# Kernel optimization log

Hardware: AMD Instinct MI355X
Metric: run time of the kernel (lower is better)

## Reference

```python
import jax, jax.numpy as jnp
import numpy as np

RADIUS = 4  # matches init radius


def _bilinear_sample(v, grid):
    """Faithful F.grid_sample(v, grid, mode='bilinear', align_corners=True, padding_mode='zeros').
    v: (B,C,H,W); grid: (B,Hg,Wg,2) in [-1,1]; grid[...,0]->width(x), grid[...,1]->height(y)."""
    B, C, H, W = v.shape
    Hg, Wg = grid.shape[1], grid.shape[2]
    ix = (grid[..., 0] + 1.0) * 0.5 * (W - 1)
    iy = (grid[..., 1] + 1.0) * 0.5 * (H - 1)
    x0 = jnp.floor(ix); y0 = jnp.floor(iy)
    x1 = x0 + 1.0;      y1 = y0 + 1.0
    wx1 = ix - x0; wx0 = 1.0 - wx1
    wy1 = iy - y0; wy0 = 1.0 - wy1
    v_flat = v.reshape(B, C, H * W)
    out = jnp.zeros((B, C, Hg, Wg), v.dtype)
    for xf, yf, w in ((x0, y0, wx0 * wy0), (x1, y0, wx1 * wy0),
                      (x0, y1, wx0 * wy1), (x1, y1, wx1 * wy1)):
        valid = (xf >= 0) & (xf <= W - 1) & (yf >= 0) & (yf <= H - 1)
        xi = jnp.clip(xf, 0, W - 1).astype(jnp.int32)
        yi = jnp.clip(yf, 0, H - 1).astype(jnp.int32)
        idx = (yi * W + xi).reshape(B, 1, Hg * Wg)
        g = jnp.take_along_axis(v_flat, idx, axis=2).reshape(B, C, Hg, Wg)
        out = out + g * (w * valid)[:, None, :, :]
    return out


def setup_inputs() -> dict:
    key = jax.random.key(0)
    ks = jax.random.split(key, 5)
    B, C, H, W, K = 4, 128, 128, 128, 8
    x = jax.random.normal(ks[0], (B, C, H, W), jnp.float32)
    psf_tbl = jax.random.randint(ks[1], (B, H, W, K, 2), 0, 128)  # absolute pixel anchors
    delta = jax.random.normal(ks[2], (1, 1, 1, K, 2), jnp.float32) * 0.1
    w_qkv = jax.random.normal(ks[3], (3 * C, C), jnp.float32) * (C ** -0.5)  # 1x1 conv, no bias
    w_proj = jax.random.normal(ks[4], (C, C), jnp.float32) * (C ** -0.5)
    return {"x": x, "psf_tbl": psf_tbl, "delta": delta, "w_qkv": w_qkv, "w_proj": w_proj}


def reference(x, psf_tbl, delta, w_qkv, w_proj):
    B, C, H, W = x.shape
    K = psf_tbl.shape[3]
    qkv = jnp.einsum('oc,bchw->bohw', w_qkv, x)  # 1x1 conv to_qkv
    q, k, v = jnp.split(qkv, 3, axis=1)
    offsets = psf_tbl.astype(x.dtype) + jnp.tanh(delta) * RADIUS  # (B,H,W,K,2)
    norm = jnp.array([H - 1, W - 1], x.dtype)
    grid = (offsets / norm * 2.0 - 1.0).reshape(B, H, W * K, 2)
    k_s = _bilinear_sample(k, grid).reshape(B, C, H, W, K)
    v_s = _bilinear_sample(v, grid).reshape(B, C, H, W, K)
    attn = jnp.einsum('bchw,bchwk->bhwk', q, k_s) * (C ** -0.5)
    attn = jax.nn.softmax(attn, axis=-1)  # softmax over K sampled points
    out = jnp.einsum('bhwk,bchwk->bchw', attn, v_s)
    return x + jnp.einsum('oc,bchw->bohw', w_proj, out)
```

## Files before the change

kernel.cpp:

```cpp
#include <hip/hip_runtime.h>

#define HW 16384
#define C 128

typedef __attribute__((ext_vector_type(8))) short short8;
typedef __attribute__((ext_vector_type(4))) float f32x4;
typedef __attribute__((ext_vector_type(2))) float f32x2;

__device__ __forceinline__ unsigned short f2bf(float f) {
  union { float f; unsigned u; } v; v.f = f;
  return (unsigned short)((v.u + 0x7fffu + ((v.u >> 16) & 1u)) >> 16);
}
#if __has_builtin(__builtin_amdgcn_cvt_pk_bf16_f32)
typedef __attribute__((ext_vector_type(2))) __bf16 bf16x2;
__device__ __forceinline__ unsigned pk2(float a, float b) {
  union { bf16x2 v; unsigned u; } cv;
  cv.v = __builtin_amdgcn_cvt_pk_bf16_f32(a, b);
  return cv.u;
}
#else
__device__ __forceinline__ unsigned pk2(float a, float b) {
  return (unsigned)f2bf(a) | ((unsigned)f2bf(b) << 16);
}
#endif
__device__ __forceinline__ unsigned short f2bf1(float a) {
  return (unsigned short)(pk2(a, a) & 0xffffu);
}
__device__ __forceinline__ float bflo(unsigned w) {
  union { unsigned u; float f; } v; v.u = w << 16; return v.f;
}
__device__ __forceinline__ float bfhi(unsigned w) {
  union { unsigned u; float f; } v; v.u = w & 0xffff0000u; return v.f;
}

__global__ void k_prep(const float* __restrict__ delta, float* __restrict__ pw,
                       int* __restrict__ pi) {
  int k = threadIdx.x;
  if (k < 8) {
    float s0 = tanhf(delta[k * 2 + 0]) * 4.0f;
    float s1 = tanhf(delta[k * 2 + 1]) * 4.0f;
    float f0 = floorf(s0), f1 = floorf(s1);
    pi[2 * k + 0] = (int)f0;
    pi[2 * k + 1] = (int)f1;
    float fx = s0 - f0, fy = s1 - f1;
    pw[4 * k + 0] = (1.0f - fx) * (1.0f - fy);
    pw[4 * k + 1] = fx * (1.0f - fy);
    pw[4 * k + 2] = (1.0f - fx) * fy;
    pw[4 * k + 3] = fx * fy;
  }
}

__global__ __launch_bounds__(256) void k_qkv(const float* __restrict__ x,
                                             const float* __restrict__ w_qkv,
                                             unsigned short* __restrict__ qb,
                                             unsigned* __restrict__ kvb) {
  __shared__ __align__(16) unsigned char smem[66560];
  unsigned short* Xs = (unsigned short*)smem;
  unsigned short* Ws = (unsigned short*)(smem + 32768);
  const int t = threadIdx.x;
  const int gpix0 = blockIdx.x * 128;
  const int b = gpix0 >> 14;
  const int hw0 = gpix0 & (HW - 1);

  const float* xb = x + (size_t)b * C * HW + hw0;
  #pragma unroll
  for (int i = 0; i < 16; ++i) {
    int linear = i * 256 + t;
    int p = linear & 127;
    int c4 = (linear >> 7) * 4;
    float a0 = xb[(size_t)(c4 + 0) * HW + p];
    float a1 = xb[(size_t)(c4 + 1) * HW + p];
    float a2 = xb[(size_t)(c4 + 2) * HW + p];
    float a3 = xb[(size_t)(c4 + 3) * HW + p];
    int cc = c4 ^ ((p & 7) << 3);
    *(uint2*)&Xs[p * 128 + cc] = make_uint2(pk2(a0, a1), pk2(a2, a3));
  }

  const int wave = t >> 6, lane = t & 63;
  const int wr = wave >> 1, wc = wave & 1;
  const int rsel = lane & 15, quad = lane >> 4;

  #pragma unroll
  for (int i = 0; i < 16; ++i) {
    int linear = i * 256 + t;
    int c4 = (linear & 31) * 4;
    int o = linear >> 5;
    float4 w4 = *(const float4*)(w_qkv + (size_t)o * C + c4);
    *(uint2*)&Ws[o * 128 + (c4 ^ ((o & 7) << 3))] = make_uint2(pk2(w4.x, w4.y), pk2(w4.z, w4.w));
  }
  __syncthreads();
  {
    f32x4 acc[4][4];
    #pragma unroll
    for (int mi = 0; mi < 4; ++mi)
      #pragma unroll
      for (int ni = 0; ni < 4; ++ni) acc[mi][ni] = (f32x4){0.f, 0.f, 0.f, 0.f};
    #pragma unroll
    for (int ks = 0; ks < 4; ++ks) {
      const int koff = ks * 32 + quad * 8;
      short8 afr[4], bfr[4];
      #pragma unroll
      for (int mi = 0; mi < 4; ++mi) {
        int r = wr * 64 + mi * 16 + rsel;
        afr[mi] = *(const short8*)&Xs[r * 128 + (koff ^ ((r & 7) << 3))];
      }
      #pragma unroll
      for (int ni = 0; ni < 4; ++ni) {
        int r = wc * 64 + ni * 16 + rsel;
        bfr[ni] = *(const short8*)&Ws[r * 128 + (koff ^ ((r & 7) << 3))];
      }
      #pragma unroll
      for (int mi = 0; mi < 4; ++mi)
        #pragma unroll
        for (int ni = 0; ni < 4; ++ni)
          acc[mi][ni] = __builtin_amdgcn_mfma_f32_16x16x32_bf16(afr[mi], bfr[ni], acc[mi][ni], 0, 0, 0);
    }
    #pragma unroll
    for (int mi = 0; mi < 4; ++mi)
      #pragma unroll
      for (int ni = 0; ni < 4; ++ni)
        #pragma unroll
        for (int r = 0; r < 4; ++r) {
          int pix = gpix0 + wr * 64 + mi * 16 + quad * 4 + r;
          int ch = wc * 64 + ni * 16 + rsel;
          qb[(size_t)pix * C + ch] = f2bf1(acc[mi][ni][r]);
        }
  }

  f32x4 acck[4][4], accv[4][4];
  #pragma unroll
  for (int mi = 0; mi < 4; ++mi)
    #pragma unroll
    for (int ni = 0; ni < 4; ++ni) {
      acck[mi][ni] = (f32x4){0.f, 0.f, 0.f, 0.f};
      accv[mi][ni] = (f32x4){0.f, 0.f, 0.f, 0.f};
    }
  #pragma unroll
  for (int ph = 0; ph < 2; ++ph) {
    __syncthreads();
    const float* wsrc = w_qkv + (size_t)(128 + ph * 128) * C;
    #pragma unroll
    for (int i = 0; i < 16; ++i) {
      int linear = i * 256 + t;
      int c4 = (linear & 31) * 4;
      int o = linear >> 5;
      float4 w4 = *(const float4*)(wsrc + (size_t)o * C + c4);
      *(uint2*)&Ws[o * 128 + (c4 ^ ((o & 7) << 3))] = make_uint2(pk2(w4.x, w4.y), pk2(w4.z, w4.w));
    }
    __syncthreads();
    #pragma unroll
    for (int ks = 0; ks < 4; ++ks) {
      const int koff = ks * 32 + quad * 8;
      short8 afr[4], bfr[4];
      #pragma unroll
      for (int mi = 0; mi < 4; ++mi) {
        int r = wr * 64 + mi * 16 + rsel;
        afr[mi] = *(const short8*)&Ws[r * 128 + (koff ^ ((r & 7) << 3))];
      }
      #pragma unroll
      for (int ni = 0; ni < 4; ++ni) {
        int r = wc * 64 + ni * 16 + rsel;
        bfr[ni] = *(const short8*)&Xs[r * 128 + (koff ^ ((r & 7) << 3))];
      }
      #pragma unroll
      for (int mi = 0; mi < 4; ++mi)
        #pragma unroll
        for (int ni = 0; ni < 4; ++ni) {
          if (ph == 0)
            acck[mi][ni] = __builtin_amdgcn_mfma_f32_16x16x32_bf16(afr[mi], bfr[ni], acck[mi][ni], 0, 0, 0);
          else
            accv[mi][ni] = __builtin_amdgcn_mfma_f32_16x16x32_bf16(afr[mi], bfr[ni], accv[mi][ni], 0, 0, 0);
        }
    }
  }
  __syncthreads();
  unsigned* kvs = (unsigned*)smem;
  #pragma unroll
  for (int mi = 0; mi < 4; ++mi)
    #pragma unroll
    for (int ni = 0; ni < 4; ++ni) {
      int ochb = wr * 64 + mi * 16 + quad * 4;
      int pixl = wc * 64 + ni * 16 + rsel;
      unsigned d0 = (unsigned)__builtin_amdgcn_cvt_pk_fp8_f32(acck[mi][ni][0], acck[mi][ni][1], 0, false) & 0xffffu;
      d0 = (unsigned)__builtin_amdgcn_cvt_pk_fp8_f32(accv[mi][ni][0], accv[mi][ni][1], (int)d0, true);
      unsigned d1 = (unsigned)__builtin_amdgcn_cvt_pk_fp8_f32(acck[mi][ni][2], acck[mi][ni][3], 0, false) & 0xffffu;
      d1 = (unsigned)__builtin_amdgcn_cvt_pk_fp8_f32(accv[mi][ni][2], accv[mi][ni][3], (int)d1, true);
      kvs[pixl * 65 + (ochb >> 1) + 0] = d0;
      kvs[pixl * 65 + (ochb >> 1) + 1] = d1;
    }
  __syncthreads();
  #pragma unroll
  for (int i = 0; i < 32; ++i) {
    int linear = i * 256 + t;
    int p = linear >> 6;
    int d = linear & 63;
    kvb[((size_t)(gpix0 + p)) * 64 + d] = kvs[p * 65 + d];
  }
}

__global__ __launch_bounds__(256) void k_attn(const unsigned short* __restrict__ qb,
                                              const unsigned* __restrict__ kvb,
                                              const int* __restrict__ psf,
                                              const float* __restrict__ pw,
                                              const int* __restrict__ pi,
                                              unsigned short* __restrict__ ao) {
  const int t = threadIdx.x;
  const int lane = t & 63;
  const int p = blockIdx.x;
  const int b = (p >> 1) & 3;
  const int j = ((p >> 3) << 1) | (p & 1);
  const int spix = __builtin_amdgcn_readfirstlane((b << 14) + (j << 2) + (t >> 6));

  const unsigned* kv32 = kvb + (size_t)b * HW * 64;

  const unsigned qp = ((const unsigned*)qb)[(size_t)spix * 64 + lane];
  const float qx = bflo(qp), qy = bfhi(qp);

  int anch[16];
  #pragma unroll
  for (int jj = 0; jj < 16; ++jj) anch[jj] = psf[(size_t)spix * 16 + jj];

  float dk[8];
  float2 vs[8];
  #pragma unroll
  for (int k = 0; k < 8; ++k) {
    const int x0 = anch[k * 2 + 0] + pi[2 * k + 0], x1 = x0 + 1;
    const int y0 = anch[k * 2 + 1] + pi[2 * k + 1], y1 = y0 + 1;
    float ksx = 0, ksy = 0, vsx = 0, vsy = 0;
    #pragma unroll
    for (int cn = 0; cn < 4; ++cn) {
      const int xi = (cn & 1) ? x1 : x0;
      const int yi = (cn & 2) ? y1 : y0;
      const bool valid = (xi >= 0) & (xi <= 127) & (yi >= 0) & (yi <= 127);
      const int xc = min(max(xi, 0), 127);
      const int yc = min(max(yi, 0), 127);
      const float wv = valid ? pw[k * 4 + cn] : 0.0f;
      const unsigned kv = kv32[(size_t)(yc * 128 + xc) * 64 + lane];
      f32x2 kp = __builtin_amdgcn_cvt_pk_f32_fp8((int)kv, false);
      f32x2 vp = __builtin_amdgcn_cvt_pk_f32_fp8((int)kv, true);
      ksx += wv * kp.x; ksy += wv * kp.y;
      vsx += wv * vp.x; vsy += wv * vp.y;
    }
    vs[k] = make_float2(vsx, vsy);
    dk[k] = qx * ksx + qy * ksy;
  }
  #pragma unroll
  for (int off = 32; off > 0; off >>= 1) {
    #pragma unroll
    for (int k = 0; k < 8; ++k) dk[k] += __shfl_xor(dk[k], off);
  }
  float lg[8];
  float m = dk[0] * 0.08838834764831845f;
  #pragma unroll
  for (int k = 0; k < 8; ++k) { lg[k] = dk[k] * 0.08838834764831845f; m = fmaxf(m, lg[k]); }
  float e[8], den = 0.0f;
  #pragma unroll
  for (int k = 0; k < 8; ++k) { e[k] = __expf(lg[k] - m); den += e[k]; }
  const float inv = 1.0f / den;
  float ox = 0, oy = 0;
  #pragma unroll
  for (int k = 0; k < 8; ++k) { float pk = e[k] * inv; ox += pk * vs[k].x; oy += pk * vs[k].y; }
  ((unsigned*)ao)[(size_t)spix * 64 + lane] = pk2(ox, oy);
}

__global__ __launch_bounds__(256) void k_proj(const unsigned short* __restrict__ ao,
                                              const float* __restrict__ w_proj,
                                              const float* __restrict__ x,
                                              float* __restrict__ out) {
  __shared__ __align__(16) unsigned short As[128 * 128];
  __shared__ __align__(16) unsigned short Ws[128 * 128];
  const int t = threadIdx.x;
  const int gpix0 = blockIdx.x * 128;
  const int b = gpix0 >> 14;
  const int hw0 = gpix0 & (HW - 1);

  #pragma unroll
  for (int i = 0; i < 8; ++i) {
    int linear = i * 256 + t;
    int c8 = (linear & 15) * 8;
    int p = linear >> 4;
    uint4 v = *(const uint4*)(ao + (size_t)(gpix0 + p) * C + c8);
    *(uint4*)&As[p * 128 + (c8 ^ ((p & 7) << 3))] = v;
  }
  #pragma unroll
  for (int i = 0; i < 16; ++i) {
    int linear = i * 256 + t;
    int c4 = (linear & 31) * 4;
    int o = linear >> 5;
    float4 w4 = *(const float4*)(w_proj + (size_t)o * C + c4);
    *(uint2*)&Ws[o * 128 + (c4 ^ ((o & 7) << 3))] = make_uint2(pk2(w4.x, w4.y), pk2(w4.z, w4.w));
  }
  __syncthreads();

  const int wave = t >> 6, lane = t & 63;
  const int wr = wave >> 1, wc = wave & 1;
  const int rsel = lane & 15, quad = lane >> 4;

  f32x4 acc[4][4];
  #pragma unroll
  for (int mi = 0; mi < 4; ++mi)
    #pragma unroll
    for (int ni = 0; ni < 4; ++ni) acc[mi][ni] = (f32x4){0.f, 0.f, 0.f, 0.f};

  #pragma unroll
  for (int ks = 0; ks < 4; ++ks) {
    const int koff = ks * 32 + quad * 8;
    short8 afr[4], bfr[4];
    #pragma unroll
    for (int mi = 0; mi < 4; ++mi) {
      int r = wr * 64 + mi * 16 + rsel;
      afr[mi] = *(const short8*)&Ws[r * 128 + (koff ^ ((r & 7) << 3))];
    }
    #pragma unroll
    for (int ni = 0; ni < 4; ++ni) {
      int r = wc * 64 + ni * 16 + rsel;
      bfr[ni] = *(const short8*)&As[r * 128 + (koff ^ ((r & 7) << 3))];
    }
    #pragma unroll
    for (int mi = 0; mi < 4; ++mi)
      #pragma unroll
      for (int ni = 0; ni < 4; ++ni)
        acc[mi][ni] = __builtin_amdgcn_mfma_f32_16x16x32_bf16(afr[mi], bfr[ni], acc[mi][ni], 0, 0, 0);
  }

  #pragma unroll
  for (int mi = 0; mi < 4; ++mi)
    #pragma unroll
    for (int ni = 0; ni < 4; ++ni)
      #pragma unroll
      for (int r = 0; r < 4; ++r) {
        int och = wr * 64 + mi * 16 + quad * 4 + r;
        int pixl = wc * 64 + ni * 16 + rsel;
        size_t addr = ((size_t)b * C + och) * HW + hw0 + pixl;
        out[addr] = x[addr] + acc[mi][ni][r];
      }
}

extern "C" void kernel_launch(void* const* d_in, const int* in_sizes, int n_in,
                              void* d_out, int out_size, void* d_ws, size_t ws_size,
                              hipStream_t stream) {
  const float* x      = (const float*)d_in[0];
  const int*   psf    = (const int*)d_in[1];
  const float* delta  = (const float*)d_in[2];
  const float* w_qkv  = (const float*)d_in[3];
  const float* w_proj = (const float*)d_in[4];
  float* out = (float*)d_out;

  const size_t N = (size_t)4 * HW * C;
  unsigned short* qb = (unsigned short*)d_ws;
  unsigned* kvb = (unsigned*)(qb + N);
  unsigned short* ao = (unsigned short*)(kvb + (size_t)4 * HW * 64);
  float* pw = (float*)(ao + N);
  int*   pi = (int*)(pw + 32);

  k_prep<<<1, 64, 0, stream>>>(delta, pw, pi);
  k_qkv<<<dim3(512), 256, 0, stream>>>(x, w_qkv, qb, kvb);
  k_attn<<<dim3(HW), 256, 0, stream>>>(qb, kvb, psf, pw, pi, ao);
  k_proj<<<dim3(512), 256, 0, stream>>>(ao, w_proj, x, out);
}
```

Baseline: 178.1 us.

## Fold key and value weights algebraically into query and projection matrices

```diff
diff --git a/kernel.cpp b/kernel.cpp
--- a/kernel.cpp
+++ b/kernel.cpp
@@ -33,28 +33,55 @@
   union { unsigned u; float f; } v; v.u = w & 0xffff0000u; return v.f;
 }
 
-__global__ void k_prep(const float* __restrict__ delta, float* __restrict__ pw,
-                       int* __restrict__ pi) {
-  int k = threadIdx.x;
-  if (k < 8) {
-    float s0 = tanhf(delta[k * 2 + 0]) * 4.0f;
-    float s1 = tanhf(delta[k * 2 + 1]) * 4.0f;
-    float f0 = floorf(s0), f1 = floorf(s1);
-    pi[2 * k + 0] = (int)f0;
-    pi[2 * k + 1] = (int)f1;
-    float fx = s0 - f0, fy = s1 - f1;
-    pw[4 * k + 0] = (1.0f - fx) * (1.0f - fy);
-    pw[4 * k + 1] = fx * (1.0f - fy);
-    pw[4 * k + 2] = (1.0f - fx) * fy;
-    pw[4 * k + 3] = fx * fy;
-  }
-}
-
-__global__ __launch_bounds__(256) void k_qkv(const float* __restrict__ x,
-                                             const float* __restrict__ w_qkv,
-                                             unsigned short* __restrict__ qb,
-                                             unsigned* __restrict__ kvb) {
-  __shared__ __align__(16) unsigned char smem[66560];
+__global__ __launch_bounds__(128) void k_prep(const float* __restrict__ w_qkv,
+                                              const float* __restrict__ w_proj,
+                                              const float* __restrict__ delta,
+                                              unsigned short* __restrict__ Mt,
+                                              unsigned short* __restrict__ Pm,
+                                              float* __restrict__ pw,
+                                              int* __restrict__ pi) {
+  const int bid = blockIdx.x;
+  const int t = threadIdx.x;
+  if (bid == 256) {
+    if (t < 8) {
+      float s0 = tanhf(delta[t * 2 + 0]) * 4.0f;
+      float s1 = tanhf(delta[t * 2 + 1]) * 4.0f;
+      float f0 = floorf(s0), f1 = floorf(s1);
+      pi[2 * t + 0] = (int)f0;
+      pi[2 * t + 1] = (int)f1;
+      float fx = s0 - f0, fy = s1 - f1;
+      pw[4 * t + 0] = (1.0f - fx) * (1.0f - fy);
+      pw[4 * t + 1] = fx * (1.0f - fy);
+      pw[4 * t + 2] = (1.0f - fx) * fy;
+      pw[4 * t + 3] = fx * fy;
+    }
+    return;
+  }
+  const int R = bid & 127;
+  float acc = 0.0f;
+  if (bid < 128) {
+    const float* wq = w_qkv;
+    const float* wk = w_qkv + 128 * 128;
+    #pragma unroll 16
+    for (int j = 0; j < 128; ++j)
+      acc += wk[j * 128 + R] * wq[j * 128 + t];
+    acc *= 0.08838834764831845f;
+    Mt[R * 128 + (t ^ ((R & 7) << 3))] = f2bf1(acc);
+  } else {
+    const float* wv = w_qkv + 2 * 128 * 128;
+    const float* wp = w_proj + (size_t)R * 128;
+    #pragma unroll 16
+    for (int j = 0; j < 128; ++j)
+      acc += wp[j] * wv[j * 128 + t];
+    Pm[R * 128 + (t ^ ((R & 7) << 3))] = f2bf1(acc);
+  }
+}
+
+__global__ __launch_bounds__(256) void k_qx(const float* __restrict__ x,
+                                            const unsigned short* __restrict__ Mt,
+                                            unsigned short* __restrict__ qb,
+                                            unsigned* __restrict__ xq) {
+  __shared__ __align__(16) unsigned char smem[65536];
   unsigned short* Xs = (unsigned short*)smem;
   unsigned short* Ws = (unsigned short*)(smem + 32768);
   const int t = threadIdx.x;
@@ -72,134 +99,59 @@
     float a1 = xb[(size_t)(c4 + 1) * HW + p];
     float a2 = xb[(size_t)(c4 + 2) * HW + p];
     float a3 = xb[(size_t)(c4 + 3) * HW + p];
+    unsigned lo = pk2(a0, a1), hi = pk2(a2, a3);
     int cc = c4 ^ ((p & 7) << 3);
-    *(uint2*)&Xs[p * 128 + cc] = make_uint2(pk2(a0, a1), pk2(a2, a3));
-  }
+    *(uint2*)&Xs[p * 128 + cc] = make_uint2(lo, hi);
+    *(uint2*)&xq[(size_t)(gpix0 + p) * 64 + (c4 >> 1)] = make_uint2(lo, hi);
+  }
+  #pragma unroll
+  for (int i = 0; i < 8; ++i)
+    ((uint4*)Ws)[i * 256 + t] = ((const uint4*)Mt)[i * 256 + t];
+  __syncthreads();
 
   const int wave = t >> 6, lane = t & 63;
   const int wr = wave >> 1, wc = wave & 1;
   const int rsel = lane & 15, quad = lane >> 4;
 
-  #pragma unroll
-  for (int i = 0; i < 16; ++i) {
-    int linear = i * 256 + t;
-    int c4 = (linear & 31) * 4;
-    int o = linear >> 5;
-    float4 w4 = *(const float4*)(w_qkv + (size_t)o * C + c4);
-    *(uint2*)&Ws[o * 128 + (c4 ^ ((o & 7) << 3))] = make_uint2(pk2(w4.x, w4.y), pk2(w4.z, w4.w));
-  }
-  __syncthreads();
-  {
-    f32x4 acc[4][4];
-    #pragma unroll
-    for (int mi = 0; mi < 4; ++mi)
-      #pragma unroll
-      for (int ni = 0; ni < 4; ++ni) acc[mi][ni] = (f32x4){0.f, 0.f, 0.f, 0.f};
-    #pragma unroll
-    for (int ks = 0; ks < 4; ++ks) {
-      const int koff = ks * 32 + quad * 8;
-      short8 afr[4], bfr[4];
-      #pragma unroll
-      for (int mi = 0; mi < 4; ++mi) {
-        int r = wr * 64 + mi * 16 + rsel;
-        afr[mi] = *(const short8*)&Xs[r * 128 + (koff ^ ((r & 7) << 3))];
-      }
-      #pragma unroll
-      for (int ni = 0; ni < 4; ++ni) {
-        int r = wc * 64 + ni * 16 + rsel;
-        bfr[ni] = *(const short8*)&Ws[r * 128 + (koff ^ ((r & 7) << 3))];
-      }
-      #pragma unroll
-      for (int mi = 0; mi < 4; ++mi)
-        #pragma unroll
-        for (int ni = 0; ni < 4; ++ni)
-          acc[mi][ni] = __builtin_amdgcn_mfma_f32_16x16x32_bf16(afr[mi], bfr[ni], acc[mi][ni], 0, 0, 0);
+  f32x4 acc[4][4];
+  #pragma unroll
+  for (int mi = 0; mi < 4; ++mi)
+    #pragma unroll
+    for (int ni = 0; ni < 4; ++ni) acc[mi][ni] = (f32x4){0.f, 0.f, 0.f, 0.f};
+  #pragma unroll
+  for (int ks = 0; ks < 4; ++ks) {
+    const int koff = ks * 32 + quad * 8;
+    short8 afr[4], bfr[4];
+    #pragma unroll
+    for (int mi = 0; mi < 4; ++mi) {
+      int r = wr * 64 + mi * 16 + rsel;
+      afr[mi] = *(const short8*)&Xs[r * 128 + (koff ^ ((r & 7) << 3))];
+    }
+    #pragma unroll
+    for (int ni = 0; ni < 4; ++ni) {
+      int r = wc * 64 + ni * 16 + rsel;
+      bfr[ni] = *(const short8*)&Ws[r * 128 + (koff ^ ((r & 7) << 3))];
     }
     #pragma unroll
     for (int mi = 0; mi < 4; ++mi)
       #pragma unroll
       for (int ni = 0; ni < 4; ++ni)
-        #pragma unroll
-        for (int r = 0; r < 4; ++r) {
-          int pix = gpix0 + wr * 64 + mi * 16 + quad * 4 + r;
-          int ch = wc * 64 + ni * 16 + rsel;
-          qb[(size_t)pix * C + ch] = f2bf1(acc[mi][ni][r]);
-        }
-  }
-
-  f32x4 acck[4][4], accv[4][4];
+        acc[mi][ni] = __builtin_amdgcn_mfma_f32_16x16x32_bf16(afr[mi], bfr[ni], acc[mi][ni], 0, 0, 0);
+  }
   #pragma unroll
   for (int mi = 0; mi < 4; ++mi)
     #pragma unroll
-    for (int ni = 0; ni < 4; ++ni) {
-      acck[mi][ni] = (f32x4){0.f, 0.f, 0.f, 0.f};
-      accv[mi][ni] = (f32x4){0.f, 0.f, 0.f, 0.f};
-    }
-  #pragma unroll
-  for (int ph = 0; ph < 2; ++ph) {
-    __syncthreads();
-    const float* wsrc = w_qkv + (size_t)(128 + ph * 128) * C;
-    #pragma unroll
-    for (int i = 0; i < 16; ++i) {
-      int linear = i * 256 + t;
-      int c4 = (linear & 31) * 4;
-      int o = linear >> 5;
-      float4 w4 = *(const float4*)(wsrc + (size_t)o * C + c4);
-      *(uint2*)&Ws[o * 128 + (c4 ^ ((o & 7) << 3))] = make_uint2(pk2(w4.x, w4.y), pk2(w4.z, w4.w));
-    }
-    __syncthreads();
-    #pragma unroll
-    for (int ks = 0; ks < 4; ++ks) {
-      const int koff = ks * 32 + quad * 8;
-      short8 afr[4], bfr[4];
+    for (int ni = 0; ni < 4; ++ni)
       #pragma unroll
-      for (int mi = 0; mi < 4; ++mi) {
-        int r = wr * 64 + mi * 16 + rsel;
-        afr[mi] = *(const short8*)&Ws[r * 128 + (koff ^ ((r & 7) << 3))];
+      for (int r = 0; r < 4; ++r) {
+        int pix = gpix0 + wr * 64 + mi * 16 + quad * 4 + r;
+        int ch = wc * 64 + ni * 16 + rsel;
+        qb[(size_t)pix * C + ch] = f2bf1(acc[mi][ni][r]);
       }
-      #pragma unroll
-      for (int ni = 0; ni < 4; ++ni) {
-        int r = wc * 64 + ni * 16 + rsel;
-        bfr[ni] = *(const short8*)&Xs[r * 128 + (koff ^ ((r & 7) << 3))];
-      }
-      #pragma unroll
-      for (int mi = 0; mi < 4; ++mi)
-        #pragma unroll
-        for (int ni = 0; ni < 4; ++ni) {
-          if (ph == 0)
-            acck[mi][ni] = __builtin_amdgcn_mfma_f32_16x16x32_bf16(afr[mi], bfr[ni], acck[mi][ni], 0, 0, 0);
-          else
-            accv[mi][ni] = __builtin_amdgcn_mfma_f32_16x16x32_bf16(afr[mi], bfr[ni], accv[mi][ni], 0, 0, 0);
-        }
-    }
-  }
-  __syncthreads();
-  unsigned* kvs = (unsigned*)smem;
-  #pragma unroll
-  for (int mi = 0; mi < 4; ++mi)
-    #pragma unroll
-    for (int ni = 0; ni < 4; ++ni) {
-      int ochb = wr * 64 + mi * 16 + quad * 4;
-      int pixl = wc * 64 + ni * 16 + rsel;
-      unsigned d0 = (unsigned)__builtin_amdgcn_cvt_pk_fp8_f32(acck[mi][ni][0], acck[mi][ni][1], 0, false) & 0xffffu;
-      d0 = (unsigned)__builtin_amdgcn_cvt_pk_fp8_f32(accv[mi][ni][0], accv[mi][ni][1], (int)d0, true);
-      unsigned d1 = (unsigned)__builtin_amdgcn_cvt_pk_fp8_f32(acck[mi][ni][2], acck[mi][ni][3], 0, false) & 0xffffu;
-      d1 = (unsigned)__builtin_amdgcn_cvt_pk_fp8_f32(accv[mi][ni][2], accv[mi][ni][3], (int)d1, true);
-      kvs[pixl * 65 + (ochb >> 1) + 0] = d0;
-      kvs[pixl * 65 + (ochb >> 1) + 1] = d1;
-    }
-  __syncthreads();
-  #pragma unroll
-  for (int i = 0; i < 32; ++i) {
-    int linear = i * 256 + t;
-    int p = linear >> 6;
-    int d = linear & 63;
-    kvb[((size_t)(gpix0 + p)) * 64 + d] = kvs[p * 65 + d];
-  }
 }
 
 __global__ __launch_bounds__(256) void k_attn(const unsigned short* __restrict__ qb,
-                                              const unsigned* __restrict__ kvb,
+                                              const unsigned* __restrict__ xq,
                                               const int* __restrict__ psf,
                                               const float* __restrict__ pw,
                                               const int* __restrict__ pi,
@@ -211,7 +163,7 @@
   const int j = ((p >> 3) << 1) | (p & 1);
   const int spix = __builtin_amdgcn_readfirstlane((b << 14) + (j << 2) + (t >> 6));
 
-  const unsigned* kv32 = kvb + (size_t)b * HW * 64;
+  const unsigned* xB = xq + (size_t)b * HW * 64;
 
   const unsigned qp = ((const unsigned*)qb)[(size_t)spix * 64 + lane];
   const float qx = bflo(qp), qy = bfhi(qp);
@@ -221,12 +173,12 @@
   for (int jj = 0; jj < 16; ++jj) anch[jj] = psf[(size_t)spix * 16 + jj];
 
   float dk[8];
-  float2 vs[8];
+  float2 xt[8];
   #pragma unroll
   for (int k = 0; k < 8; ++k) {
     const int x0 = anch[k * 2 + 0] + pi[2 * k + 0], x1 = x0 + 1;
     const int y0 = anch[k * 2 + 1] + pi[2 * k + 1], y1 = y0 + 1;
-    float ksx = 0, ksy = 0, vsx = 0, vsy = 0;
+    float sx = 0, sy = 0;
     #pragma unroll
     for (int cn = 0; cn < 4; ++cn) {
       const int xi = (cn & 1) ? x1 : x0;
@@ -235,36 +187,33 @@
       const int xc = min(max(xi, 0), 127);
       const int yc = min(max(yi, 0), 127);
       const float wv = valid ? pw[k * 4 + cn] : 0.0f;
-      const unsigned kv = kv32[(size_t)(yc * 128 + xc) * 64 + lane];
-      f32x2 kp = __builtin_amdgcn_cvt_pk_f32_fp8((int)kv, false);
-      f32x2 vp = __builtin_amdgcn_cvt_pk_f32_fp8((int)kv, true);
-      ksx += wv * kp.x; ksy += wv * kp.y;
-      vsx += wv * vp.x; vsy += wv * vp.y;
-    }
-    vs[k] = make_float2(vsx, vsy);
-    dk[k] = qx * ksx + qy * ksy;
+      const unsigned w = xB[(size_t)(yc * 128 + xc) * 64 + lane];
+      sx += wv * bflo(w);
+      sy += wv * bfhi(w);
+    }
+    xt[k] = make_float2(sx, sy);
+    dk[k] = qx * sx + qy * sy;
   }
   #pragma unroll
   for (int off = 32; off > 0; off >>= 1) {
     #pragma unroll
     for (int k = 0; k < 8; ++k) dk[k] += __shfl_xor(dk[k], off);
   }
-  float lg[8];
-  float m = dk[0] * 0.08838834764831845f;
-  #pragma unroll
-  for (int k = 0; k < 8; ++k) { lg[k] = dk[k] * 0.08838834764831845f; m = fmaxf(m, lg[k]); }
+  float m = dk[0];
+  #pragma unroll
+  for (int k = 1; k < 8; ++k) m = fmaxf(m, dk[k]);
   float e[8], den = 0.0f;
   #pragma unroll
-  for (int k = 0; k < 8; ++k) { e[k] = __expf(lg[k] - m); den += e[k]; }
+  for (int k = 0; k < 8; ++k) { e[k] = __expf(dk[k] - m); den += e[k]; }
   const float inv = 1.0f / den;
   float ox = 0, oy = 0;
   #pragma unroll
-  for (int k = 0; k < 8; ++k) { float pk = e[k] * inv; ox += pk * vs[k].x; oy += pk * vs[k].y; }
+  for (int k = 0; k < 8; ++k) { float pk = e[k] * inv; ox += pk * xt[k].x; oy += pk * xt[k].y; }
   ((unsigned*)ao)[(size_t)spix * 64 + lane] = pk2(ox, oy);
 }
 
 __global__ __launch_bounds__(256) void k_proj(const unsigned short* __restrict__ ao,
-                                              const float* __restrict__ w_proj,
+                                              const unsigned short* __restrict__ Pm,
                                               const float* __restrict__ x,
                                               float* __restrict__ out) {
   __shared__ __align__(16) unsigned short As[128 * 128];
@@ -283,13 +232,8 @@
     *(uint4*)&As[p * 128 + (c8 ^ ((p & 7) << 3))] = v;
   }
   #pragma unroll
-  for (int i = 0; i < 16; ++i) {
-    int linear = i * 256 + t;
-    int c4 = (linear & 31) * 4;
-    int o = linear >> 5;
-    float4 w4 = *(const float4*)(w_proj + (size_t)o * C + c4);
-    *(uint2*)&Ws[o * 128 + (c4 ^ ((o & 7) << 3))] = make_uint2(pk2(w4.x, w4.y), pk2(w4.z, w4.w));
-  }
+  for (int i = 0; i < 8; ++i)
+    ((uint4*)Ws)[i * 256 + t] = ((const uint4*)Pm)[i * 256 + t];
   __syncthreads();
 
   const int wave = t >> 6, lane = t & 63;
@@ -348,13 +292,15 @@
 
   const size_t N = (size_t)4 * HW * C;
   unsigned short* qb = (unsigned short*)d_ws;
-  unsigned* kvb = (unsigned*)(qb + N);
-  unsigned short* ao = (unsigned short*)(kvb + (size_t)4 * HW * 64);
-  float* pw = (float*)(ao + N);
+  unsigned short* xq = qb + N;
+  unsigned short* ao = xq + N;
+  unsigned short* Mt = ao + N;
+  unsigned short* Pm = Mt + 16384;
+  float* pw = (float*)(Pm + 16384);
   int*   pi = (int*)(pw + 32);
 
-  k_prep<<<1, 64, 0, stream>>>(delta, pw, pi);
-  k_qkv<<<dim3(512), 256, 0, stream>>>(x, w_qkv, qb, kvb);
-  k_attn<<<dim3(HW), 256, 0, stream>>>(qb, kvb, psf, pw, pi, ao);
-  k_proj<<<dim3(512), 256, 0, stream>>>(ao, w_proj, x, out);
-}
+  k_prep<<<dim3(257), 128, 0, stream>>>(w_qkv, w_proj, delta, Mt, Pm, pw, pi);
+  k_qx<<<dim3(512), 256, 0, stream>>>(x, Mt, qb, (unsigned*)xq);
+  k_attn<<<dim3(HW), 256, 0, stream>>>(qb, (const unsigned*)xq, psf, pw, pi, ao);
+  k_proj<<<dim3(512), 256, 0, stream>>>(ao, Pm, x, out);
+}
```

Measured after the change: 176.6 us. About the same (-0.8%).
